# Kernel optimization log

Measured on AMD Instinct MI355X. Metric: run time of the kernel, lower is better.

## Reference

```python
import jax, jax.numpy as jnp
import numpy as np

N_HEAD = 12
N_EMBD = 768
HEAD_DIM = N_EMBD // N_HEAD


def setup_inputs() -> dict:
    key = jax.random.key(0)
    k1, k2, k3, k4, k5 = jax.random.split(key, 5)
    B, T, C = 1, 4096, N_EMBD
    s = 0.02
    return {
        "x": jax.random.normal(k1, (B, T, C), dtype=jnp.float32),
        "W_qkv": jax.random.normal(k2, (C, 3 * C), dtype=jnp.float32) * s,
        "b_qkv": jnp.zeros((3 * C,), dtype=jnp.float32),
        "W_out": jax.random.normal(k3, (C, C), dtype=jnp.float32) * s,
        "b_out": jnp.zeros((C,), dtype=jnp.float32),
    }


def reference(x, W_qkv, b_qkv, W_out, b_out):
    B, T, C = x.shape
    H, D = N_HEAD, HEAD_DIM
    qkv = x @ W_qkv + b_qkv                       # (B, T, 3C)
    qkv = qkv.reshape(B, T, 3, H, D)
    q = jnp.transpose(qkv[:, :, 0], (0, 2, 1, 3))  # (B, H, T, D)
    k = jnp.transpose(qkv[:, :, 1], (0, 2, 1, 3))
    v = jnp.transpose(qkv[:, :, 2], (0, 2, 1, 3))
    scores = jnp.einsum("bhqd,bhkd->bhqk", q, k) / jnp.sqrt(jnp.float32(D))
    causal = jnp.tril(jnp.ones((T, T), dtype=bool))
    scores = jnp.where(causal[None, None], scores, -jnp.inf)
    weights = jax.nn.softmax(scores, axis=-1)     # (B, H, T, T)
    out = jnp.einsum("bhqk,bhkd->bhqd", weights, v)
    out = jnp.transpose(out, (0, 2, 1, 3)).reshape(B, T, C)
    return out @ W_out + b_out
```

## Files before the change

kernel.cpp:

```cpp
#include <hip/hip_runtime.h>
#include <hip/hip_bf16.h>
#include <stdint.h>

#define T_SEQ 4096
#define C_EMB 768
#define C3    2304
#define CQK   1536
#define NH    12
#define HD    64
#define CH    16
#define NSLOT 1728

typedef __attribute__((ext_vector_type(8))) short short8;
typedef __attribute__((ext_vector_type(4))) short short4v;
typedef __attribute__((ext_vector_type(4))) float f32x4;

__device__ __forceinline__ short f2bf(float f) {
  __bf16 h = (__bf16)f;
  return __builtin_bit_cast(short, h);
}

__device__ __forceinline__ void gload_lds16(const void* g, void* l) {
  __builtin_amdgcn_global_load_lds((const __attribute__((address_space(1))) void*)g,
                                   (__attribute__((address_space(3))) void*)l, 16, 0, 0);
}

__global__ __launch_bounds__(256)
void cvt_kernel(const float* __restrict__ in, short* __restrict__ out, int n4) {
  int i = blockIdx.x * 256 + threadIdx.x;
  if (i < n4) {
    float4 v = ((const float4*)in)[i];
    short4v s = { f2bf(v.x), f2bf(v.y), f2bf(v.z), f2bf(v.w) };
    ((short4v*)out)[i] = s;
  }
}

__global__ __launch_bounds__(256)
void transpose_cvt_kernel(const float* __restrict__ W, short* __restrict__ WT,
                          int K, int N) {
  __shared__ float ts[32][33];
  const int r0 = blockIdx.y * 32, c0 = blockIdx.x * 32;
  const int tid = threadIdx.x;
  {
    int rr = tid >> 3, c4 = (tid & 7) * 4;
    float4 v = *(const float4*)(W + (size_t)(r0 + rr) * N + c0 + c4);
    ts[rr][c4 + 0] = v.x; ts[rr][c4 + 1] = v.y;
    ts[rr][c4 + 2] = v.z; ts[rr][c4 + 3] = v.w;
  }
  __syncthreads();
  {
    int nr = tid >> 3, k4 = (tid & 7) * 4;
    short4v s = { f2bf(ts[k4 + 0][nr]), f2bf(ts[k4 + 1][nr]),
                  f2bf(ts[k4 + 2][nr]), f2bf(ts[k4 + 3][nr]) };
    *(short4v*)(WT + (size_t)(c0 + nr) * K + r0 + k4) = s;
  }
}

template<int BN, bool SPLIT_V, bool OUT_F32>
__global__ __launch_bounds__(256)
void gemm_kernel(const short* __restrict__ A, const short* __restrict__ Bt,
                 const float* __restrict__ bias, void* __restrict__ Cp,
                 short* __restrict__ Vt, int N, int K) {
  constexpr int MF = (BN == 128) ? 4 : 2;
  __shared__ short As[128 * 32];
  __shared__ short Bs[BN * 32];
  const int row0 = blockIdx.y * 128, col0 = blockIdx.x * BN;
  const int tid = threadIdx.x, lane = tid & 63, wave = tid >> 6;
  const int lg = lane >> 4, lr = lane & 15;
  const int wr = (BN == 128) ? ((wave >> 1) * 64) : (wave * 32);
  const int wc = (BN == 128) ? ((wave & 1) * 64) : 0;

  f32x4 acc[MF][4];
  #pragma unroll
  for (int m_ = 0; m_ < MF; ++m_)
    #pragma unroll
    for (int n_ = 0; n_ < 4; ++n_) acc[m_][n_] = (f32x4){0.f, 0.f, 0.f, 0.f};

  const int srow = wave * 16 + (lane >> 2);
  const int scol = (lane & 3) * 8;

  for (int kt = 0; kt < K; kt += 32) {
    __syncthreads();
    #pragma unroll
    for (int c = 0; c < 2; ++c)
      gload_lds16(A + (size_t)(row0 + c * 64 + srow) * K + kt + scol,
                  As + c * 2048 + wave * 512);
    #pragma unroll
    for (int c = 0; c < BN / 64; ++c)
      gload_lds16(Bt + (size_t)(col0 + c * 64 + srow) * K + kt + scol,
                  Bs + c * 2048 + wave * 512);
    __syncthreads();

    short8 a[MF], b[4];
    #pragma unroll
    for (int m_ = 0; m_ < MF; ++m_)
      a[m_] = *(const short8*)&As[(wr + m_ * 16 + lr) * 32 + lg * 8];
    #pragma unroll
    for (int n_ = 0; n_ < 4; ++n_)
      b[n_] = *(const short8*)&Bs[(wc + n_ * 16 + lr) * 32 + lg * 8];
    #pragma unroll
    for (int m_ = 0; m_ < MF; ++m_)
      #pragma unroll
      for (int n_ = 0; n_ < 4; ++n_)
        acc[m_][n_] = __builtin_amdgcn_mfma_f32_16x16x32_bf16(a[m_], b[n_], acc[m_][n_], 0, 0, 0);
  }

  const bool isV = SPLIT_V && (col0 >= CQK);
  #pragma unroll
  for (int n_ = 0; n_ < 4; ++n_) {
    const int col = col0 + wc + n_ * 16 + lr;
    const float bv = bias[col];
    #pragma unroll
    for (int m_ = 0; m_ < MF; ++m_) {
      const int rbase = row0 + wr + m_ * 16 + lg * 4;
      if constexpr (OUT_F32) {
        #pragma unroll
        for (int r = 0; r < 4; ++r)
          ((float*)Cp)[(size_t)(rbase + r) * N + col] = acc[m_][n_][r] + bv;
      } else {
        if (!isV) {
          const int nout = SPLIT_V ? CQK : N;
          #pragma unroll
          for (int r = 0; r < 4; ++r)
            ((short*)Cp)[(size_t)(rbase + r) * nout + col] = f2bf(acc[m_][n_][r] + bv);
        } else {
          short4v p = { f2bf(acc[m_][n_][0] + bv), f2bf(acc[m_][n_][1] + bv),
                        f2bf(acc[m_][n_][2] + bv), f2bf(acc[m_][n_][3] + bv) };
          const int t64 = rbase & 63;
          const int p64 = (t64 & 32) + ((t64 & 12) << 1) + ((t64 & 16) >> 2);
          *(short4v*)(Vt + (size_t)(col - CQK) * T_SEQ + (rbase & ~63) + p64) = p;
        }
      }
    }
  }
}

__global__ __launch_bounds__(512, 4)
void attn_kernel(const short* __restrict__ qk, const short* __restrict__ Vt,
                 short* __restrict__ out, float* __restrict__ pO,
                 float* __restrict__ pML) {
  __shared__ short smem[18432];
  const int bd = blockIdx.x;
  const int h = bd % NH;
  const int ii = 159 - bd / NH;
  int qt, ck;
  if (ii < 16)      { qt = ii;                 ck = 0; }
  else if (ii < 48) { qt = 16 + (ii - 16) / 2; ck = (ii - 16) % 2; }
  else if (ii < 96) { qt = 32 + (ii - 48) / 3; ck = (ii - 48) % 3; }
  else              { qt = 48 + (ii - 96) / 4; ck = (ii - 96) % 4; }
  const int q0 = qt * 64;
  const int ntiles = qt + 1;
  const int t0 = ck * CH;
  const int rem = ntiles - t0;
  const int nloc = rem < CH ? rem : CH;

  const int tid = threadIdx.x, lane = tid & 63, wave = tid >> 6;
  const int st = wave >> 2, qslot = wave & 3;
  const int lg = lane >> 4, lr = lane & 15;
  const int q = q0 + qslot * 16 + lr;
  const float SC = 0.18033688011f;

  short (*Ks)[72] = (short(*)[72])(smem + st * 4608);
  short (*Vs)[72] = (short(*)[72])(smem + 9216 + st * 4608);

  short8 qf[2];
  qf[0] = *(const short8*)(qk + (size_t)q * CQK + h * HD + lg * 8);
  qf[1] = *(const short8*)(qk + (size_t)q * CQK + h * HD + 32 + lg * 8);

  float mrun = -1e30f, lrun = 0.f;
  f32x4 o[4];
  #pragma unroll
  for (int d = 0; d < 4; ++d) o[d] = (f32x4){0.f, 0.f, 0.f, 0.f};

  const int srow = qslot * 16 + (lane >> 3);
  const int scol = (lane & 7) * 8;
  const short* Kg = qk + C_EMB + h * HD;
  const short* Vg = Vt + (size_t)(h * HD) * T_SEQ;

  const int nO = nloc >> 1, nE = nloc - nO;
  const int nMine = st ? nO : nE;

  if (nMine > 0) {
    const int kt = (t0 + st) * 64;
    #pragma unroll
    for (int p = 0; p < 2; ++p) {
      const int r = srow + 8 * p;
      *(short8*)&Ks[r][scol] = *(const short8*)(Kg + (size_t)(kt + r) * CQK + scol);
      *(short8*)&Vs[r][scol] = *(const short8*)(Vg + (size_t)r * T_SEQ + kt + scol);
    }
  }
  __syncthreads();

  for (int tt = 0; tt < nE; ++tt) {
    const bool haveNext = (tt + 1 < nMine);
    short8 kr[2], vr[2];
    if (haveNext) {
      const int kt = (t0 + 2 * (tt + 1) + st) * 64;
      #pragma unroll
      for (int p = 0; p < 2; ++p) {
        const int r = srow + 8 * p;
        kr[p] = *(const short8*)(Kg + (size_t)(kt + r) * CQK + scol);
        vr[p] = *(const short8*)(Vg + (size_t)r * T_SEQ + kt + scol);
      }
    }

    if (tt < nMine) {
      const int tl = t0 + 2 * tt + st;
      f32x4 s[4];
      __builtin_amdgcn_s_setprio(1);
      #pragma unroll
      for (int n = 0; n < 4; ++n) {
        f32x4 cc = (f32x4){0.f, 0.f, 0.f, 0.f};
        #pragma unroll
        for (int ks = 0; ks < 2; ++ks) {
          short8 kb = *(const short8*)&Ks[n * 16 + lr][ks * 32 + lg * 8];
          cc = __builtin_amdgcn_mfma_f32_16x16x32_bf16(kb, qf[ks], cc, 0, 0, 0);
        }
        s[n] = cc;
      }
      __builtin_amdgcn_s_setprio(0);

      if (tl == ntiles - 1) {
        #pragma unroll
        for (int n = 0; n < 4; ++n)
          #pragma unroll
          for (int r = 0; r < 4; ++r)
            if (n * 16 + lg * 4 + r > qslot * 16 + lr) s[n][r] = -1e30f;
      }

      float pmax = s[0][0];
      #pragma unroll
      for (int n = 0; n < 4; ++n)
        #pragma unroll
        for (int r = 0; r < 4; ++r) pmax = fmaxf(pmax, s[n][r]);
      pmax = fmaxf(pmax, __shfl_xor(pmax, 16));
      pmax = fmaxf(pmax, __shfl_xor(pmax, 32));

      if (!__all(pmax <= mrun + 44.0f)) {
        const float mn = fmaxf(mrun, pmax);
        const float al = exp2f((mrun - mn) * SC);
        lrun *= al;
        #pragma unroll
        for (int d = 0; d < 4; ++d) o[d] *= al;
        mrun = mn;
      }
      const float msc = mrun * SC;

      float psum = 0.f;
      #pragma unroll
      for (int n = 0; n < 4; ++n)
        #pragma unroll
        for (int r = 0; r < 4; ++r) {
          float p = exp2f(fmaf(s[n][r], SC, -msc));
          s[n][r] = p;
          psum += p;
        }
      psum += __shfl_xor(psum, 16);
      psum += __shfl_xor(psum, 32);
      lrun += psum;

      __builtin_amdgcn_s_setprio(1);
      #pragma unroll
      for (int ks = 0; ks < 2; ++ks) {
        short8 pb = { f2bf(s[2 * ks][0]),     f2bf(s[2 * ks][1]),
                      f2bf(s[2 * ks][2]),     f2bf(s[2 * ks][3]),
                      f2bf(s[2 * ks + 1][0]), f2bf(s[2 * ks + 1][1]),
                      f2bf(s[2 * ks + 1][2]), f2bf(s[2 * ks + 1][3]) };
        #pragma unroll
        for (int d = 0; d < 4; ++d) {
          short8 av = *(const short8*)&Vs[d * 16 + lr][ks * 32 + lg * 8];
          o[d] = __builtin_amdgcn_mfma_f32_16x16x32_bf16(av, pb, o[d], 0, 0, 0);
        }
      }
      __builtin_amdgcn_s_setprio(0);
    }

    __syncthreads();
    if (haveNext) {
      #pragma unroll
      for (int p = 0; p < 2; ++p) {
        const int r = srow + 8 * p;
        *(short8*)&Ks[r][scol] = kr[p];
        *(short8*)&Vs[r][scol] = vr[p];
      }
    }
    __syncthreads();
  }

  float* mo = (float*)smem;
  float* ml = (float*)((char*)smem + 17408);
  if (st == 1) {
    const int row = qslot * 16 + lr;
    #pragma unroll
    for (int d = 0; d < 4; ++d)
      *(f32x4*)&mo[row * 68 + d * 16 + lg * 4] = o[d];
    if (lg == 0) {
      ml[row * 2 + 0] = mrun;
      ml[row * 2 + 1] = lrun;
    }
  }
  __syncthreads();
  if (st == 0) {
    const int row = qslot * 16 + lr;
    const float mb = ml[row * 2 + 0], lb = ml[row * 2 + 1];
    const float M = fmaxf(mrun, mb);
    const float aa = exp2f((mrun - M) * SC);
    const float ab = exp2f((mb - M) * SC);
    const float lmerged = lrun * aa + lb * ab;
    if (qt < CH) {
      const float linv = 1.f / lmerged;
      #pragma unroll
      for (int d = 0; d < 4; ++d) {
        f32x4 ob = *(const f32x4*)&mo[row * 68 + d * 16 + lg * 4];
        short4v ov;
        #pragma unroll
        for (int r = 0; r < 4; ++r)
          ov[r] = f2bf((o[d][r] * aa + ob[r] * ab) * linv);
        *(short4v*)(out + (size_t)q * C_EMB + h * HD + d * 16 + lg * 4) = ov;
      }
    } else {
      const int sbase = (qt < 32) ? 2 * (qt - 16)
                      : (qt < 48) ? 32 + 3 * (qt - 32)
                                  : 80 + 4 * (qt - 48);
      const int slot = h * 144 + sbase + ck;
      float* po = pO + (size_t)slot * 4096 + row * 64;
      #pragma unroll
      for (int d = 0; d < 4; ++d) {
        f32x4 ob = *(const f32x4*)&mo[row * 68 + d * 16 + lg * 4];
        f32x4 v;
        #pragma unroll
        for (int r = 0; r < 4; ++r) v[r] = o[d][r] * aa + ob[r] * ab;
        *(f32x4*)&po[d * 16 + lg * 4] = v;
      }
      if (lg == 0) {
        pML[(size_t)slot * 128 + row * 2 + 0] = M;
        pML[(size_t)slot * 128 + row * 2 + 1] = lmerged;
      }
    }
  }
}

__global__ __launch_bounds__(256)
void merge_kernel(const float* __restrict__ pO, const float* __restrict__ pML,
                  short* __restrict__ out) {
  const int bd = blockIdx.x;
  const int h = bd % NH;
  const int qt = 16 + bd / NH;
  const int nc = qt / CH + 1;
  const int sbase = (qt < 32) ? 2 * (qt - 16)
                  : (qt < 48) ? 32 + 3 * (qt - 32)
                              : 80 + 4 * (qt - 48);
  const int slot0 = h * 144 + sbase;
  const int tid = threadIdx.x;
  const int q = tid >> 2, dc = (tid & 3) << 4;
  const float SC = 0.18033688011f;

  float mi[4], li[4];
  float M = -1e30f;
  #pragma unroll
  for (int i = 0; i < 4; ++i)
    if (i < nc) {
      mi[i] = pML[(size_t)(slot0 + i) * 128 + q * 2 + 0];
      li[i] = pML[(size_t)(slot0 + i) * 128 + q * 2 + 1];
      M = fmaxf(M, mi[i]);
    }

  f32x4 O[4];
  #pragma unroll
  for (int d4 = 0; d4 < 4; ++d4) O[d4] = (f32x4){0.f, 0.f, 0.f, 0.f};
  float L = 0.f;
  #pragma unroll
  for (int i = 0; i < 4; ++i)
    if (i < nc) {
      const float a = exp2f((mi[i] - M) * SC);
      L = fmaf(li[i], a, L);
      const float* po = pO + (size_t)(slot0 + i) * 4096 + q * 64 + dc;
      #pragma unroll
      for (int d4 = 0; d4 < 4; ++d4) {
        f32x4 v = *(const f32x4*)(po + d4 * 4);
        #pragma unroll
        for (int r = 0; r < 4; ++r) O[d4][r] = fmaf(v[r], a, O[d4][r]);
      }
    }

  const float linv = 1.f / L;
  #pragma unroll
  for (int d4 = 0; d4 < 4; ++d4) {
    short4v ov;
    #pragma unroll
    for (int r = 0; r < 4; ++r) ov[r] = f2bf(O[d4][r] * linv);
    *(short4v*)(out + (size_t)(qt * 64 + q) * C_EMB + h * HD + dc + d4 * 4) = ov;
  }
}

extern "C" void kernel_launch(void* const* d_in, const int* in_sizes, int n_in,
                              void* d_out, int out_size, void* d_ws, size_t ws_size,
                              hipStream_t stream) {
  const float* x    = (const float*)d_in[0];
  const float* Wqkv = (const float*)d_in[1];
  const float* bqkv = (const float*)d_in[2];
  const float* Wout = (const float*)d_in[3];
  const float* bout = (const float*)d_in[4];

  short* xb    = (short*)d_ws;
  short* WqkvT = xb    + (size_t)T_SEQ * C_EMB;
  short* WoutT = WqkvT + (size_t)C3 * C_EMB;
  short* qk    = WoutT + (size_t)C_EMB * C_EMB;
  short* Vt    = qk    + (size_t)T_SEQ * CQK;
  float* pO    = (float*)(Vt + (size_t)C_EMB * T_SEQ);
  float* pML   = pO + (size_t)NSLOT * 4096;

  cvt_kernel<<<(T_SEQ * C_EMB / 4) / 256, 256, 0, stream>>>(x, xb, T_SEQ * C_EMB / 4);
  transpose_cvt_kernel<<<dim3(C3 / 32, C_EMB / 32), 256, 0, stream>>>(Wqkv, WqkvT, C_EMB, C3);
  transpose_cvt_kernel<<<dim3(C_EMB / 32, C_EMB / 32), 256, 0, stream>>>(Wout, WoutT, C_EMB, C_EMB);

  gemm_kernel<128, true, false><<<dim3(C3 / 128, T_SEQ / 128), 256, 0, stream>>>(
      xb, WqkvT, bqkv, qk, Vt, C3, C_EMB);

  attn_kernel<<<dim3(NH * 160), 512, 0, stream>>>(qk, Vt, xb, pO, pML);
  merge_kernel<<<dim3(NH * 48), 256, 0, stream>>>(pO, pML, xb);

  gemm_kernel<64, false, true><<<dim3(C_EMB / 64, T_SEQ / 128), 256, 0, stream>>>(
      xb, WoutT, bout, d_out, nullptr, C_EMB, C_EMB);
}
```

Measured before the change: 140.7 us.

## Restructure attention so each wave owns a full 64-row query chunk, loading K/V straight to registers

The attention kernel moves from 512-thread blocks, where two wave groups split the K tiles through shared memory and then merge their partial results, to one wave per (head, query tile, chunk) work item. Each wave holds all four 16-row query groups and reads K and V fragments directly from global memory into registers. This removes LDS staging, the block-wide barriers and the in-block merge. In exchange each wave keeps far more registers live (64 accumulator floats plus the K/V fragments), gets less parallelism per work item, and loses the software prefetch, so global load latency is exposed each iteration.

```diff
diff --git a/kernel.cpp b/kernel.cpp
--- a/kernel.cpp
+++ b/kernel.cpp
@@ -135,14 +135,14 @@
   }
 }
 
-__global__ __launch_bounds__(512, 4)
+__global__ __launch_bounds__(256, 2)
 void attn_kernel(const short* __restrict__ qk, const short* __restrict__ Vt,
                  short* __restrict__ out, float* __restrict__ pO,
                  float* __restrict__ pML) {
-  __shared__ short smem[18432];
-  const int bd = blockIdx.x;
-  const int h = bd % NH;
-  const int ii = 159 - bd / NH;
+  const int w = blockIdx.x * 4 + (threadIdx.x >> 6);
+  const int lane = threadIdx.x & 63;
+  const int h = w % NH;
+  const int ii = 159 - w / NH;
   int qt, ck;
   if (ii < 16)      { qt = ii;                 ck = 0; }
   else if (ii < 48) { qt = 16 + (ii - 16) / 2; ck = (ii - 16) % 2; }
@@ -154,68 +154,59 @@
   const int rem = ntiles - t0;
   const int nloc = rem < CH ? rem : CH;
 
-  const int tid = threadIdx.x, lane = tid & 63, wave = tid >> 6;
-  const int st = wave >> 2, qslot = wave & 3;
   const int lg = lane >> 4, lr = lane & 15;
-  const int q = q0 + qslot * 16 + lr;
   const float SC = 0.18033688011f;
 
-  short (*Ks)[72] = (short(*)[72])(smem + st * 4608);
-  short (*Vs)[72] = (short(*)[72])(smem + 9216 + st * 4608);
-
-  short8 qf[2];
-  qf[0] = *(const short8*)(qk + (size_t)q * CQK + h * HD + lg * 8);
-  qf[1] = *(const short8*)(qk + (size_t)q * CQK + h * HD + 32 + lg * 8);
-
-  float mrun = -1e30f, lrun = 0.f;
-  f32x4 o[4];
-  #pragma unroll
-  for (int d = 0; d < 4; ++d) o[d] = (f32x4){0.f, 0.f, 0.f, 0.f};
-
-  const int srow = qslot * 16 + (lane >> 3);
-  const int scol = (lane & 7) * 8;
-  const short* Kg = qk + C_EMB + h * HD;
-  const short* Vg = Vt + (size_t)(h * HD) * T_SEQ;
-
-  const int nO = nloc >> 1, nE = nloc - nO;
-  const int nMine = st ? nO : nE;
-
-  if (nMine > 0) {
-    const int kt = (t0 + st) * 64;
-    #pragma unroll
-    for (int p = 0; p < 2; ++p) {
-      const int r = srow + 8 * p;
-      *(short8*)&Ks[r][scol] = *(const short8*)(Kg + (size_t)(kt + r) * CQK + scol);
-      *(short8*)&Vs[r][scol] = *(const short8*)(Vg + (size_t)r * T_SEQ + kt + scol);
-    }
-  }
-  __syncthreads();
-
-  for (int tt = 0; tt < nE; ++tt) {
-    const bool haveNext = (tt + 1 < nMine);
-    short8 kr[2], vr[2];
-    if (haveNext) {
-      const int kt = (t0 + 2 * (tt + 1) + st) * 64;
-      #pragma unroll
-      for (int p = 0; p < 2; ++p) {
-        const int r = srow + 8 * p;
-        kr[p] = *(const short8*)(Kg + (size_t)(kt + r) * CQK + scol);
-        vr[p] = *(const short8*)(Vg + (size_t)r * T_SEQ + kt + scol);
-      }
-    }
-
-    if (tt < nMine) {
-      const int tl = t0 + 2 * tt + st;
+  short8 qf[4][2];
+  #pragma unroll
+  for (int g = 0; g < 4; ++g)
+    #pragma unroll
+    for (int ks = 0; ks < 2; ++ks)
+      qf[g][ks] = *(const short8*)(qk + (size_t)(q0 + g * 16 + lr) * CQK +
+                                   h * HD + ks * 32 + lg * 8);
+
+  float mrun[4], lrun[4];
+  f32x4 o[4][4];
+  #pragma unroll
+  for (int g = 0; g < 4; ++g) { mrun[g] = -1e30f; lrun[g] = 0.f; }
+  #pragma unroll
+  for (int d = 0; d < 4; ++d)
+    #pragma unroll
+    for (int g = 0; g < 4; ++g) o[d][g] = (f32x4){0.f, 0.f, 0.f, 0.f};
+
+  const short* kp[4];
+  const short* vp[4];
+  #pragma unroll
+  for (int n = 0; n < 4; ++n)
+    kp[n] = qk + C_EMB + h * HD + (size_t)(t0 * 64 + n * 16 + lr) * CQK + lg * 8;
+  #pragma unroll
+  for (int d = 0; d < 4; ++d)
+    vp[d] = Vt + (size_t)(h * HD + d * 16 + lr) * T_SEQ + t0 * 64 + lg * 8;
+
+  for (int tt = 0; tt < nloc; ++tt) {
+    const int tl = t0 + tt;
+
+    short8 kf[4][2], vf[4][2];
+    #pragma unroll
+    for (int n = 0; n < 4; ++n) {
+      kf[n][0] = *(const short8*)(kp[n]);
+      kf[n][1] = *(const short8*)(kp[n] + 32);
+      vf[n][0] = *(const short8*)(vp[n]);
+      vf[n][1] = *(const short8*)(vp[n] + 32);
+      kp[n] += 64 * CQK;
+      vp[n] += 64;
+    }
+
+    #pragma unroll
+    for (int g = 0; g < 4; ++g) {
       f32x4 s[4];
       __builtin_amdgcn_s_setprio(1);
       #pragma unroll
       for (int n = 0; n < 4; ++n) {
         f32x4 cc = (f32x4){0.f, 0.f, 0.f, 0.f};
         #pragma unroll
-        for (int ks = 0; ks < 2; ++ks) {
-          short8 kb = *(const short8*)&Ks[n * 16 + lr][ks * 32 + lg * 8];
-          cc = __builtin_amdgcn_mfma_f32_16x16x32_bf16(kb, qf[ks], cc, 0, 0, 0);
-        }
+        for (int ks = 0; ks < 2; ++ks)
+          cc = __builtin_amdgcn_mfma_f32_16x16x32_bf16(kf[n][ks], qf[g][ks], cc, 0, 0, 0);
         s[n] = cc;
       }
       __builtin_amdgcn_s_setprio(0);
@@ -225,7 +216,7 @@
         for (int n = 0; n < 4; ++n)
           #pragma unroll
           for (int r = 0; r < 4; ++r)
-            if (n * 16 + lg * 4 + r > qslot * 16 + lr) s[n][r] = -1e30f;
+            if (n * 16 + lg * 4 + r > g * 16 + lr) s[n][r] = -1e30f;
       }
 
       float pmax = s[0][0];
@@ -236,15 +227,15 @@
       pmax = fmaxf(pmax, __shfl_xor(pmax, 16));
       pmax = fmaxf(pmax, __shfl_xor(pmax, 32));
 
-      if (!__all(pmax <= mrun + 44.0f)) {
-        const float mn = fmaxf(mrun, pmax);
-        const float al = exp2f((mrun - mn) * SC);
-        lrun *= al;
-        #pragma unroll
-        for (int d = 0; d < 4; ++d) o[d] *= al;
-        mrun = mn;
-      }
-      const float msc = mrun * SC;
+      if (!__all(pmax <= mrun[g] + 44.0f)) {
+        const float mn = fmaxf(mrun[g], pmax);
+        const float al = exp2f((mrun[g] - mn) * SC);
+        lrun[g] *= al;
+        #pragma unroll
+        for (int d = 0; d < 4; ++d) o[d][g] *= al;
+        mrun[g] = mn;
+      }
+      const float msc = mrun[g] * SC;
 
       float psum = 0.f;
       #pragma unroll
@@ -257,7 +248,7 @@
         }
       psum += __shfl_xor(psum, 16);
       psum += __shfl_xor(psum, 32);
-      lrun += psum;
+      lrun[g] += psum;
 
       __builtin_amdgcn_s_setprio(1);
       #pragma unroll
@@ -267,74 +258,41 @@
                       f2bf(s[2 * ks + 1][0]), f2bf(s[2 * ks + 1][1]),
                       f2bf(s[2 * ks + 1][2]), f2bf(s[2 * ks + 1][3]) };
         #pragma unroll
-        for (int d = 0; d < 4; ++d) {
-          short8 av = *(const short8*)&Vs[d * 16 + lr][ks * 32 + lg * 8];
-          o[d] = __builtin_amdgcn_mfma_f32_16x16x32_bf16(av, pb, o[d], 0, 0, 0);
-        }
+        for (int d = 0; d < 4; ++d)
+          o[d][g] = __builtin_amdgcn_mfma_f32_16x16x32_bf16(vf[d][ks], pb, o[d][g], 0, 0, 0);
       }
       __builtin_amdgcn_s_setprio(0);
     }
-
-    __syncthreads();
-    if (haveNext) {
-      #pragma unroll
-      for (int p = 0; p < 2; ++p) {
-        const int r = srow + 8 * p;
-        *(short8*)&Ks[r][scol] = kr[p];
-        *(short8*)&Vs[r][scol] = vr[p];
-      }
-    }
-    __syncthreads();
-  }
-
-  float* mo = (float*)smem;
-  float* ml = (float*)((char*)smem + 17408);
-  if (st == 1) {
-    const int row = qslot * 16 + lr;
-    #pragma unroll
-    for (int d = 0; d < 4; ++d)
-      *(f32x4*)&mo[row * 68 + d * 16 + lg * 4] = o[d];
-    if (lg == 0) {
-      ml[row * 2 + 0] = mrun;
-      ml[row * 2 + 1] = lrun;
-    }
-  }
-  __syncthreads();
-  if (st == 0) {
-    const int row = qslot * 16 + lr;
-    const float mb = ml[row * 2 + 0], lb = ml[row * 2 + 1];
-    const float M = fmaxf(mrun, mb);
-    const float aa = exp2f((mrun - M) * SC);
-    const float ab = exp2f((mb - M) * SC);
-    const float lmerged = lrun * aa + lb * ab;
-    if (qt < CH) {
-      const float linv = 1.f / lmerged;
+  }
+
+  if (qt < CH) {
+    #pragma unroll
+    for (int g = 0; g < 4; ++g) {
+      const float linv = 1.f / lrun[g];
+      const size_t qrow = q0 + g * 16 + lr;
       #pragma unroll
       for (int d = 0; d < 4; ++d) {
-        f32x4 ob = *(const f32x4*)&mo[row * 68 + d * 16 + lg * 4];
         short4v ov;
         #pragma unroll
-        for (int r = 0; r < 4; ++r)
-          ov[r] = f2bf((o[d][r] * aa + ob[r] * ab) * linv);
-        *(short4v*)(out + (size_t)q * C_EMB + h * HD + d * 16 + lg * 4) = ov;
-      }
-    } else {
-      const int sbase = (qt < 32) ? 2 * (qt - 16)
-                      : (qt < 48) ? 32 + 3 * (qt - 32)
-                                  : 80 + 4 * (qt - 48);
-      const int slot = h * 144 + sbase + ck;
+        for (int r = 0; r < 4; ++r) ov[r] = f2bf(o[d][g][r] * linv);
+        *(short4v*)(out + qrow * C_EMB + h * HD + d * 16 + lg * 4) = ov;
+      }
+    }
+  } else {
+    const int sbase = (qt < 32) ? 2 * (qt - 16)
+                    : (qt < 48) ? 32 + 3 * (qt - 32)
+                                : 80 + 4 * (qt - 48);
+    const int slot = h * 144 + sbase + ck;
+    #pragma unroll
+    for (int g = 0; g < 4; ++g) {
+      const int row = g * 16 + lr;
       float* po = pO + (size_t)slot * 4096 + row * 64;
       #pragma unroll
-      for (int d = 0; d < 4; ++d) {
-        f32x4 ob = *(const f32x4*)&mo[row * 68 + d * 16 + lg * 4];
-        f32x4 v;
-        #pragma unroll
-        for (int r = 0; r < 4; ++r) v[r] = o[d][r] * aa + ob[r] * ab;
-        *(f32x4*)&po[d * 16 + lg * 4] = v;
-      }
+      for (int d = 0; d < 4; ++d)
+        *(f32x4*)&po[d * 16 + lg * 4] = o[d][g];
       if (lg == 0) {
-        pML[(size_t)slot * 128 + row * 2 + 0] = M;
-        pML[(size_t)slot * 128 + row * 2 + 1] = lmerged;
+        pML[(size_t)slot * 128 + row * 2 + 0] = mrun[g];
+        pML[(size_t)slot * 128 + row * 2 + 1] = lrun[g];
       }
     }
   }
@@ -417,7 +375,7 @@
   gemm_kernel<128, true, false><<<dim3(C3 / 128, T_SEQ / 128), 256, 0, stream>>>(
       xb, WqkvT, bqkv, qk, Vt, C3, C_EMB);
 
-  attn_kernel<<<dim3(NH * 160), 512, 0, stream>>>(qk, Vt, xb, pO, pML);
+  attn_kernel<<<dim3(480), 256, 0, stream>>>(qk, Vt, xb, pO, pML);
   merge_kernel<<<dim3(NH * 48), 256, 0, stream>>>(pO, pML, xb);
 
   gemm_kernel<64, false, true><<<dim3(C_EMB / 64, T_SEQ / 128), 256, 0, stream>>>(
```

Result: no change. 140.8 us (+0.1%).
